# Performance work log

Hardware: AMD Instinct MI355X
Metric: run time of the kernel (lower is better)

Reference implementation:

```python
import jax, jax.numpy as jnp
import numpy as np
import math

B, T, D, H = 2, 2048, 1024, 16
HD = D // H


def setup_inputs() -> dict:
    key = jax.random.key(0)
    k1, k2, k3 = jax.random.split(key, 3)
    x = jax.random.normal(k1, (B, T, D), dtype=jnp.float32)
    attn_mask = jnp.ones((B, T), dtype=jnp.int32)
    W_qkv = jax.random.normal(k2, (D, 3 * D), dtype=jnp.float32) * (1.0 / math.sqrt(D))
    W_out = jax.random.normal(k3, (D, D), dtype=jnp.float32) * (1.0 / math.sqrt(D))
    return {"x": x, "attn_mask": attn_mask, "W_qkv": W_qkv, "W_out": W_out}


def reference(x, attn_mask, W_qkv, W_out):
    Bx, Tx, Dx = x.shape
    qkv = jnp.einsum("btd,de->bte", x, W_qkv)  # (B,T,3D)
    q, k, v = jnp.split(qkv, 3, axis=-1)
    # (B,T,D) -> (B,H,T,hd)
    q = q.reshape(Bx, Tx, H, HD).transpose(0, 2, 1, 3)
    k = k.reshape(Bx, Tx, H, HD).transpose(0, 2, 1, 3)
    v = v.reshape(Bx, Tx, H, HD).transpose(0, 2, 1, 3)
    scale = 1.0 / math.sqrt(HD)
    scores = jnp.einsum("bhqd,bhkd->bhqk", q, k) * scale  # (B,H,T,T)
    # padding mask over keys: (B,T) -> (B,1,1,T)
    mask = attn_mask[:, None, None, :]
    scores = jnp.where(mask == 0, jnp.float32(-jnp.inf), scores)
    attn = jax.nn.softmax(scores, axis=-1)
    out = jnp.einsum("bhqk,bhkd->bhqd", attn, v)  # (B,H,T,hd)
    out = out.transpose(0, 2, 1, 3).reshape(Bx, Tx, Dx)
    return jnp.einsum("btd,de->bte", out, W_out)
```

## Files before the change

kernel.cpp:

```cpp
#include <hip/hip_runtime.h>

#define B_ 2
#define T_ 2048
#define D_ 1024
#define H_ 16
#define HD_ 64
#define NT_ (B_*T_)

typedef __attribute__((ext_vector_type(8))) short bf16x8;
typedef __attribute__((ext_vector_type(4))) float f32x4;
typedef __attribute__((ext_vector_type(16))) float f32x16;
typedef __attribute__((ext_vector_type(4))) int i32x4;

#define MFMA32(a, b, c) __builtin_amdgcn_mfma_f32_32x32x16_bf16((a), (b), (c), 0, 0, 0)

static __device__ __forceinline__ unsigned short f2bf(float f) {
    union { float f; unsigned u; } v; v.f = f;
    unsigned r = v.u + 0x7fffu + ((v.u >> 16) & 1u);
    return (unsigned short)(r >> 16);
}

static __device__ __forceinline__ float exp2a(float x) {
    float r; asm("v_exp_f32 %0, %1" : "=v"(r) : "v"(x)); return r;
}

static __device__ __forceinline__ unsigned cvt_pk_bf16(float lo, float hi) {
    unsigned r; asm("v_cvt_pk_bf16_f32 %0, %1, %2" : "=v"(r) : "v"(lo), "v"(hi)); return r;
}

static __device__ __forceinline__ void gload_lds16(const unsigned short* g, unsigned short* l) {
    __builtin_amdgcn_global_load_lds(
        (const __attribute__((address_space(1))) unsigned int*)g,
        (__attribute__((address_space(3))) unsigned int*)l, 16, 0, 0);
}

static __device__ __forceinline__ void xcd_swz(int& bx, int& by) {
    int gx = gridDim.x, nwg = gx * gridDim.y;
    int flat = by * gx + bx;
    int cpx = nwg >> 3;
    int swz = (flat & 7) * cpx + (flat >> 3);
    bx = swz % gx; by = swz / gx;
}

__global__ __launch_bounds__(256) void cast_f32_bf16(
    const float* __restrict__ in, unsigned short* __restrict__ out, int n) {
    int base = (blockIdx.x * blockDim.x + threadIdx.x) * 8;
    if (base >= n) return;
    f32x4 a = *(const f32x4*)(in + base);
    f32x4 b = *(const f32x4*)(in + base + 4);
    unsigned short o[8];
#pragma unroll
    for (int j = 0; j < 4; ++j) { o[j] = f2bf(a[j]); o[j + 4] = f2bf(b[j]); }
    *(i32x4*)(out + base) = *(const i32x4*)o;
}

__global__ __launch_bounds__(256) void transpose_cast(
    const float* __restrict__ in, unsigned short* __restrict__ out, int R, int C) {
    __shared__ float tile[32][33];
    int c0 = blockIdx.x * 32, r0 = blockIdx.y * 32;
    int tx = threadIdx.x, ty = threadIdx.y;
#pragma unroll
    for (int j = 0; j < 32; j += 8)
        tile[ty + j][tx] = in[(size_t)(r0 + ty + j) * C + c0 + tx];
    __syncthreads();
#pragma unroll
    for (int j = 0; j < 32; j += 8)
        out[(size_t)(c0 + ty + j) * R + r0 + tx] = f2bf(tile[tx][ty + j]);
}

template <int EPI>
__global__ __launch_bounds__(256) void gemm_bt(
    const unsigned short* __restrict__ A, const unsigned short* __restrict__ Bt,
    float* __restrict__ C,
    unsigned short* __restrict__ Qo, unsigned short* __restrict__ Ko,
    unsigned short* __restrict__ Vo,
    int M, int N, int K) {
    __shared__ __align__(16) unsigned short As[128 * 64];
    __shared__ __align__(16) unsigned short Bs[128 * 64];
    int tid = threadIdx.x;
    int wv = tid >> 6, lane = tid & 63;
    int wr = wv >> 1, wc = wv & 1;
    int l15 = lane & 15, lg = lane >> 4;
    int bx = blockIdx.x, by = blockIdx.y;
    xcd_swz(bx, by);
    int tm = by * 128, tn = bx * 128;
    f32x4 acc[4][4] = {};

    int lrow = lane >> 3;
    int scol = ((lane & 7) ^ (lrow & 7)) * 8;
    int rsw = l15 & 7;

    for (int kt = 0; kt < K; kt += 64) {
        __syncthreads();
#pragma unroll
        for (int c = 0; c < 4; ++c) {
            int chunk = wv + c * 4;
            gload_lds16(A + (size_t)(tm + chunk * 8 + lrow) * K + kt + scol, As + chunk * 512);
            gload_lds16(Bt + (size_t)(tn + chunk * 8 + lrow) * K + kt + scol, Bs + chunk * 512);
        }
        __syncthreads();
#pragma unroll
        for (int kk = 0; kk < 2; ++kk) {
            bf16x8 af[4], bfr[4];
#pragma unroll
            for (int m = 0; m < 4; ++m) {
                int row = wr * 64 + m * 16 + l15;
                af[m] = *(const bf16x8*)(As + row * 64 + (((kk * 4 + lg) ^ rsw) * 8));
            }
#pragma unroll
            for (int n = 0; n < 4; ++n) {
                int row = wc * 64 + n * 16 + l15;
                bfr[n] = *(const bf16x8*)(Bs + row * 64 + (((kk * 4 + lg) ^ rsw) * 8));
            }
#pragma unroll
            for (int m = 0; m < 4; ++m)
#pragma unroll
                for (int n = 0; n < 4; ++n)
                    acc[m][n] = __builtin_amdgcn_mfma_f32_16x16x32_bf16(af[m], bfr[n], acc[m][n], 0, 0, 0);
        }
    }

    if (EPI == 0) {
#pragma unroll
        for (int m = 0; m < 4; ++m) {
            int row0 = tm + wr * 64 + m * 16 + lg * 4;
#pragma unroll
            for (int n = 0; n < 4; ++n) {
                int col = tn + wc * 64 + n * 16 + l15;
#pragma unroll
                for (int r = 0; r < 4; ++r)
                    C[(size_t)(row0 + r) * N + col] = acc[m][n][r];
            }
        }
    } else {
        const float SC = 0.125f * 1.44269504f;
#pragma unroll
        for (int m = 0; m < 4; ++m) {
            int row0 = tm + wr * 64 + m * 16 + lg * 4;
#pragma unroll
            for (int n = 0; n < 4; ++n) {
                int e = tn + wc * 64 + n * 16 + l15;
                int sec = e >> 10, rem = e & 1023;
                int h = rem >> 6, hd = rem & 63;
                int tok = row0;
                int b = tok >> 11, tl = tok & 2047;
                if (sec == 2) {
                    size_t idx0 = ((size_t)(b * H_ + h) * HD_ + hd) * T_ + tl;
                    *(unsigned*)(Vo + idx0)     = cvt_pk_bf16(acc[m][n][0], acc[m][n][1]);
                    *(unsigned*)(Vo + idx0 + 2) = cvt_pk_bf16(acc[m][n][2], acc[m][n][3]);
                } else {
                    unsigned short* dst = (sec == 0) ? Qo : Ko;
                    float sc = (sec == 0) ? SC : 1.0f;
#pragma unroll
                    for (int r = 0; r < 4; ++r)
                        dst[(((size_t)(b * H_ + h) * T_ + tl + r) << 6) + hd] =
                            f2bf(acc[m][n][r] * sc);
                }
            }
        }
    }
}

#define KPAD 72
#define VPAD 136

#define EXCH(PV, HF, FRAG)                                                     \
  do {                                                                         \
    unsigned uA0 = cvt_pk_bf16(PV[8 * HF + 0], PV[8 * HF + 1]);                \
    unsigned uA1 = cvt_pk_bf16(PV[8 * HF + 2], PV[8 * HF + 3]);                \
    unsigned uB0 = cvt_pk_bf16(PV[8 * HF + 4], PV[8 * HF + 5]);                \
    unsigned uB1 = cvt_pk_bf16(PV[8 * HF + 6], PV[8 * HF + 7]);                \
    unsigned snd0 = hi ? uA0 : uB0, snd1 = hi ? uA1 : uB1;                     \
    unsigned rc0 = (unsigned)__shfl_xor((int)snd0, 32);                        \
    unsigned rc1 = (unsigned)__shfl_xor((int)snd1, 32);                        \
    union { bf16x8 v; unsigned u[4]; } Fx;                                     \
    Fx.u[0] = hi ? rc0 : uA0;                                                  \
    Fx.u[1] = hi ? rc1 : uA1;                                                  \
    Fx.u[2] = hi ? uB0 : rc0;                                                  \
    Fx.u[3] = hi ? uB1 : rc1;                                                  \
    FRAG = Fx.v;                                                               \
  } while (0)

__global__ __launch_bounds__(256) void flash_attn(
    const unsigned short* __restrict__ Qg, const unsigned short* __restrict__ Kg,
    const unsigned short* __restrict__ VTg, const int* __restrict__ mask,
    unsigned short* __restrict__ AO) {
    __shared__ __align__(16) unsigned short Ks[128 * KPAD];
    __shared__ __align__(16) unsigned short VTs[64 * VPAD];
    __shared__ float biasS[128];

    int tid = threadIdx.x, wv = tid >> 6, lane = tid & 63;
    int l31 = lane & 31, hi = lane >> 5;
    int bx = blockIdx.x, by = blockIdx.y;
    xcd_swz(bx, by);
    int bh = by;
    int b = bh >> 4, h = bh & 15;
    int q0 = bx * 128;
    const unsigned short* Qb  = Qg  + (size_t)bh * T_ * HD_;
    const unsigned short* Kb  = Kg  + (size_t)bh * T_ * HD_;
    const unsigned short* VTb = VTg + (size_t)bh * HD_ * T_;

    bf16x8 qf[4];
    {
        const unsigned short* qrow = Qb + (size_t)(q0 + wv * 32 + l31) * HD_;
#pragma unroll
        for (int c = 0; c < 4; ++c)
            qf[c] = *(const bf16x8*)(qrow + c * 16 + hi * 8);
    }

    float lp0 = 0.f, lp1 = 0.f, lp2 = 0.f, lp3 = 0.f;
    f32x16 o0 = {}, o1 = {};

    i32x4 kv[4], vvv[4];
#pragma unroll
    for (int c = 0; c < 4; ++c) {
        int idx = tid + c * 256;
        kv[c]  = *(const i32x4*)(Kb + (size_t)(idx >> 3) * HD_ + (idx & 7) * 8);
        vvv[c] = *(const i32x4*)(VTb + (size_t)(idx >> 4) * T_ + (idx & 15) * 8);
    }
    int mA = mask[b * T_ + lane];
    int mB = mask[b * T_ + 64 + lane];

    for (int kt = 0; kt < T_; kt += 128) {
        bool nomask = __all(mA != 0 && mB != 0);
        __syncthreads();
#pragma unroll
        for (int c = 0; c < 4; ++c) {
            int idx = tid + c * 256;
            *(i32x4*)(Ks + (idx >> 3) * KPAD + (idx & 7) * 8) = kv[c];
            *(i32x4*)(VTs + (idx >> 4) * VPAD + (idx & 15) * 8) = vvv[c];
        }
        if (!nomask && wv == 0) {
            biasS[lane]      = mA ? 0.f : -1e30f;
            biasS[64 + lane] = mB ? 0.f : -1e30f;
        }
        if (kt + 128 < T_) {
#pragma unroll
            for (int c = 0; c < 4; ++c) {
                int idx = tid + c * 256;
                kv[c]  = *(const i32x4*)(Kb + (size_t)(kt + 128 + (idx >> 3)) * HD_ + (idx & 7) * 8);
                vvv[c] = *(const i32x4*)(VTb + (size_t)(idx >> 4) * T_ + kt + 128 + (idx & 15) * 8);
            }
            mA = mask[b * T_ + kt + 128 + lane];
            mB = mask[b * T_ + kt + 192 + lane];
        }
        __syncthreads();

#pragma unroll
        for (int hp = 0; hp < 2; ++hp) {
            f32x16 s0 = {}, s1 = {};
            __builtin_amdgcn_s_setprio(1);
#pragma unroll
            for (int c = 0; c < 4; ++c) {
                bf16x8 ka = *(const bf16x8*)(Ks + ((hp * 2 + 0) * 32 + l31) * KPAD + c * 16 + hi * 8);
                s0 = MFMA32(ka, qf[c], s0);
            }
#pragma unroll
            for (int c = 0; c < 4; ++c) {
                bf16x8 kb2 = *(const bf16x8*)(Ks + ((hp * 2 + 1) * 32 + l31) * KPAD + c * 16 + hi * 8);
                s1 = MFMA32(kb2, qf[c], s1);
            }
            __builtin_amdgcn_s_setprio(0);

            if (!nomask) {
#pragma unroll
                for (int i = 0; i < 16; ++i) {
                    int krow = (i & 3) + 8 * (i >> 2) + 4 * hi;
                    s0[i] += biasS[hp * 64 + krow];
                    s1[i] += biasS[hp * 64 + 32 + krow];
                }
            }
#pragma unroll
            for (int i = 0; i < 16; i += 4) {
                s0[i] = exp2a(s0[i]);     s0[i+1] = exp2a(s0[i+1]);
                s0[i+2] = exp2a(s0[i+2]); s0[i+3] = exp2a(s0[i+3]);
                s1[i] = exp2a(s1[i]);     s1[i+1] = exp2a(s1[i+1]);
                s1[i+2] = exp2a(s1[i+2]); s1[i+3] = exp2a(s1[i+3]);
                lp0 += s0[i]   + s1[i];
                lp1 += s0[i+1] + s1[i+1];
                lp2 += s0[i+2] + s1[i+2];
                lp3 += s0[i+3] + s1[i+3];
            }
            bf16x8 fr0, fr1, fr2, fr3;
            EXCH(s0, 0, fr0);
            EXCH(s0, 1, fr1);
            EXCH(s1, 0, fr2);
            EXCH(s1, 1, fr3);

            __builtin_amdgcn_s_setprio(1);
#pragma unroll
            for (int kc = 0; kc < 4; ++kc) {
                bf16x8 fr = (kc == 0) ? fr0 : (kc == 1) ? fr1 : (kc == 2) ? fr2 : fr3;
                bf16x8 va = *(const bf16x8*)(VTs + l31 * VPAD + hp * 64 + kc * 16 + hi * 8);
                bf16x8 vb = *(const bf16x8*)(VTs + (32 + l31) * VPAD + hp * 64 + kc * 16 + hi * 8);
                o0 = MFMA32(fr, va, o0);
                o1 = MFMA32(fr, vb, o1);
            }
            __builtin_amdgcn_s_setprio(0);
        }
    }

    float l_part = (lp0 + lp1) + (lp2 + lp3);
    l_part += __shfl_xor(l_part, 32);

    size_t rowD = (size_t)(b * T_ + q0 + wv * 32) * D_ + h * 64;
#pragma unroll
    for (int i = 0; i < 16; ++i) {
        int qrow = (i & 3) + 8 * (i >> 2) + 4 * hi;
        float lq = __shfl(l_part, qrow);
        float inv = 1.0f / lq;
        AO[rowD + (size_t)qrow * D_ + l31]      = f2bf(o0[i] * inv);
        AO[rowD + (size_t)qrow * D_ + 32 + l31] = f2bf(o1[i] * inv);
    }
}

extern "C" void kernel_launch(void* const* d_in, const int* in_sizes, int n_in,
                              void* d_out, int out_size, void* d_ws, size_t ws_size,
                              hipStream_t stream) {
    const float* x    = (const float*)d_in[0];
    const int*   mask = (const int*)d_in[1];
    const float* Wqkv = (const float*)d_in[2];
    const float* Wout = (const float*)d_in[3];
    float* out = (float*)d_out;
    char* ws = (char*)d_ws;

    unsigned short* Xb    = (unsigned short*)(ws);
    unsigned short* WqkvT = (unsigned short*)(ws + (size_t)(8u << 20));
    unsigned short* WoutT = (unsigned short*)(ws + (size_t)(14u << 20));
    unsigned short* Qg    = (unsigned short*)(ws + (size_t)(16u << 20));
    unsigned short* Kg    = (unsigned short*)(ws + (size_t)(24u << 20));
    unsigned short* VT    = (unsigned short*)(ws + (size_t)(32u << 20));
    unsigned short* AO    = Xb;

    cast_f32_bf16<<<2048, 256, 0, stream>>>(x, Xb, NT_ * D_);
    transpose_cast<<<dim3(3072 / 32, 1024 / 32), dim3(32, 8), 0, stream>>>(Wqkv, WqkvT, 1024, 3072);
    transpose_cast<<<dim3(1024 / 32, 1024 / 32), dim3(32, 8), 0, stream>>>(Wout, WoutT, 1024, 1024);
    gemm_bt<1><<<dim3(3072 / 128, 4096 / 128), 256, 0, stream>>>(
        Xb, WqkvT, nullptr, Qg, Kg, VT, NT_, 3 * D_, D_);
    flash_attn<<<dim3(T_ / 128, B_ * H_), 256, 0, stream>>>(Qg, Kg, VT, mask, AO);
    gemm_bt<0><<<dim3(1024 / 128, 4096 / 128), 256, 0, stream>>>(
        AO, WoutT, out, nullptr, nullptr, nullptr, NT_, D_, D_);
}
```

Before: 136.6 us.

## Merge prep kernels into one launch and use 128x64 tiles for output GEMM

```diff
diff --git a/kernel.cpp b/kernel.cpp
--- a/kernel.cpp
+++ b/kernel.cpp
@@ -42,23 +42,32 @@
     bx = swz % gx; by = swz / gx;
 }
 
-__global__ __launch_bounds__(256) void cast_f32_bf16(
-    const float* __restrict__ in, unsigned short* __restrict__ out, int n) {
-    int base = (blockIdx.x * blockDim.x + threadIdx.x) * 8;
-    if (base >= n) return;
-    f32x4 a = *(const f32x4*)(in + base);
-    f32x4 b = *(const f32x4*)(in + base + 4);
-    unsigned short o[8];
-#pragma unroll
-    for (int j = 0; j < 4; ++j) { o[j] = f2bf(a[j]); o[j + 4] = f2bf(b[j]); }
-    *(i32x4*)(out + base) = *(const i32x4*)o;
-}
-
-__global__ __launch_bounds__(256) void transpose_cast(
-    const float* __restrict__ in, unsigned short* __restrict__ out, int R, int C) {
+__global__ __launch_bounds__(256) void prep_all(
+    const float* __restrict__ x, unsigned short* __restrict__ Xb,
+    const float* __restrict__ Wqkv, unsigned short* __restrict__ WqkvT,
+    const float* __restrict__ Wout, unsigned short* __restrict__ WoutT) {
     __shared__ float tile[32][33];
-    int c0 = blockIdx.x * 32, r0 = blockIdx.y * 32;
-    int tx = threadIdx.x, ty = threadIdx.y;
+    int bid = blockIdx.x, tid = threadIdx.x;
+    if (bid < 2048) {
+        int base = (bid * 256 + tid) * 8;
+        f32x4 a = *(const f32x4*)(x + base);
+        f32x4 b = *(const f32x4*)(x + base + 4);
+        unsigned short o[8];
+#pragma unroll
+        for (int j = 0; j < 4; ++j) { o[j] = f2bf(a[j]); o[j + 4] = f2bf(b[j]); }
+        *(i32x4*)(Xb + base) = *(const i32x4*)o;
+        return;
+    }
+    const float* in; unsigned short* out; int R, C, bx, by;
+    if (bid < 5120) {
+        int tb = bid - 2048; bx = tb % 96; by = tb / 96;
+        in = Wqkv; out = WqkvT; R = 1024; C = 3072;
+    } else {
+        int tb = bid - 5120; bx = tb & 31; by = tb >> 5;
+        in = Wout; out = WoutT; R = 1024; C = 1024;
+    }
+    int tx = tid & 31, ty = tid >> 5;
+    int c0 = bx * 32, r0 = by * 32;
 #pragma unroll
     for (int j = 0; j < 32; j += 8)
         tile[ty + j][tx] = in[(size_t)(r0 + ty + j) * C + c0 + tx];
@@ -161,6 +170,71 @@
     }
 }
 
+__global__ __launch_bounds__(256) void gemm_n64(
+    const unsigned short* __restrict__ A, const unsigned short* __restrict__ Bt,
+    float* __restrict__ C, int M, int N, int K) {
+    __shared__ __align__(16) unsigned short As[128 * 64];
+    __shared__ __align__(16) unsigned short Bs[64 * 64];
+    int tid = threadIdx.x;
+    int wv = tid >> 6, lane = tid & 63;
+    int wr = wv >> 1, wc = wv & 1;
+    int l15 = lane & 15, lg = lane >> 4;
+    int bx = blockIdx.x, by = blockIdx.y;
+    xcd_swz(bx, by);
+    int tm = by * 128, tn = bx * 64;
+    f32x4 acc[4][2] = {};
+
+    int lrow = lane >> 3;
+    int scol = ((lane & 7) ^ (lrow & 7)) * 8;
+    int rsw = l15 & 7;
+
+    for (int kt = 0; kt < K; kt += 64) {
+        __syncthreads();
+#pragma unroll
+        for (int c = 0; c < 4; ++c) {
+            int chunk = wv + c * 4;
+            gload_lds16(A + (size_t)(tm + chunk * 8 + lrow) * K + kt + scol, As + chunk * 512);
+        }
+#pragma unroll
+        for (int c = 0; c < 2; ++c) {
+            int chunk = wv + c * 4;
+            gload_lds16(Bt + (size_t)(tn + chunk * 8 + lrow) * K + kt + scol, Bs + chunk * 512);
+        }
+        __syncthreads();
+#pragma unroll
+        for (int kk = 0; kk < 2; ++kk) {
+            bf16x8 af[4], bfr[2];
+#pragma unroll
+            for (int m = 0; m < 4; ++m) {
+                int row = wr * 64 + m * 16 + l15;
+                af[m] = *(const bf16x8*)(As + row * 64 + (((kk * 4 + lg) ^ rsw) * 8));
+            }
+#pragma unroll
+            for (int n = 0; n < 2; ++n) {
+                int row = wc * 32 + n * 16 + l15;
+                bfr[n] = *(const bf16x8*)(Bs + row * 64 + (((kk * 4 + lg) ^ rsw) * 8));
+            }
+#pragma unroll
+            for (int m = 0; m < 4; ++m)
+#pragma unroll
+                for (int n = 0; n < 2; ++n)
+                    acc[m][n] = __builtin_amdgcn_mfma_f32_16x16x32_bf16(af[m], bfr[n], acc[m][n], 0, 0, 0);
+        }
+    }
+
+#pragma unroll
+    for (int m = 0; m < 4; ++m) {
+        int row0 = tm + wr * 64 + m * 16 + lg * 4;
+#pragma unroll
+        for (int n = 0; n < 2; ++n) {
+            int col = tn + wc * 32 + n * 16 + l15;
+#pragma unroll
+            for (int r = 0; r < 4; ++r)
+                C[(size_t)(row0 + r) * N + col] = acc[m][n][r];
+        }
+    }
+}
+
 #define KPAD 72
 #define VPAD 136
 
@@ -332,12 +406,10 @@
     unsigned short* VT    = (unsigned short*)(ws + (size_t)(32u << 20));
     unsigned short* AO    = Xb;
 
-    cast_f32_bf16<<<2048, 256, 0, stream>>>(x, Xb, NT_ * D_);
-    transpose_cast<<<dim3(3072 / 32, 1024 / 32), dim3(32, 8), 0, stream>>>(Wqkv, WqkvT, 1024, 3072);
-    transpose_cast<<<dim3(1024 / 32, 1024 / 32), dim3(32, 8), 0, stream>>>(Wout, WoutT, 1024, 1024);
+    prep_all<<<6144, 256, 0, stream>>>(x, Xb, Wqkv, WqkvT, Wout, WoutT);
     gemm_bt<1><<<dim3(3072 / 128, 4096 / 128), 256, 0, stream>>>(
         Xb, WqkvT, nullptr, Qg, Kg, VT, NT_, 3 * D_, D_);
     flash_attn<<<dim3(T_ / 128, B_ * H_), 256, 0, stream>>>(Qg, Kg, VT, mask, AO);
-    gemm_bt<0><<<dim3(1024 / 128, 4096 / 128), 256, 0, stream>>>(
-        AO, WoutT, out, nullptr, nullptr, nullptr, NT_, D_, D_);
-}
+    gemm_n64<<<dim3(1024 / 64, 4096 / 128), 256, 0, stream>>>(
+        AO, WoutT, out, NT_, D_, D_);
+}
```

Result: faster. 127.7 us (-6.6%).
